# Performance work log

Measured on AMD Instinct MI355X. Metric: run time of the kernel, lower is better.

Reference implementation:

```python
import jax, jax.numpy as jnp
import numpy as np

N, E, B = 30000, 240000, 64
F, H, T = 64, 4, 3
BOT = 256


def _gat_layer(x, e_src, e_dst, lin_w, att_src, att_dst, bias):
    # x: [N, in]; lin_w: [in, H*F]; att_*: [H, F]; bias: [H*F]
    xs = (x @ lin_w).reshape(N, H, F)                     # [N,H,F]
    a_src = jnp.einsum('nhf,hf->nh', xs, att_src)         # [N,H]
    a_dst = jnp.einsum('nhf,hf->nh', xs, att_dst)
    logits = jax.nn.leaky_relu(a_src[e_src] + a_dst[e_dst], negative_slope=0.2)  # [E2,H]
    m = jax.ops.segment_max(logits, e_dst, num_segments=N)        # softmax over in-edges per dst
    ex = jnp.exp(logits - m[e_dst])
    denom = jax.ops.segment_sum(ex, e_dst, num_segments=N)
    alpha = ex / (denom[e_dst] + 1e-16)                   # [E2,H]
    msg = alpha[:, :, None] * xs[e_src]                   # [E2,H,F]
    out = jax.ops.segment_sum(msg, e_dst, num_segments=N).reshape(N, H * F)
    return out + bias


def setup_inputs() -> dict:
    key = jax.random.key(0)
    ks = jax.random.split(key, 20)
    s = 0.1
    inp = {
        'street_feature': jax.random.normal(ks[0], (N, 5), jnp.float32),
        'edge_index': jax.random.randint(ks[1], (2, E), 0, N, dtype=jnp.int64),
        'batch': jnp.sort(jax.random.randint(ks[2], (N,), 0, B, dtype=jnp.int64)),
        'bbox_w': jax.random.normal(ks[3], (5, F), jnp.float32) * s,
        'bbox_b': jnp.zeros((F,), jnp.float32),
        'lin_w0': jax.random.normal(ks[4], (F, H * F), jnp.float32) * s,
        'att_src0': jax.random.normal(ks[5], (H, F), jnp.float32) * s,
        'att_dst0': jax.random.normal(ks[6], (H, F), jnp.float32) * s,
        'bias0': jnp.zeros((H * F,), jnp.float32),
        'lin_w1': jax.random.normal(ks[7], (H * F, H * F), jnp.float32) * s,
        'att_src1': jax.random.normal(ks[8], (H, F), jnp.float32) * s,
        'att_dst1': jax.random.normal(ks[9], (H, F), jnp.float32) * s,
        'bias1': jnp.zeros((H * F,), jnp.float32),
        'lin_w2': jax.random.normal(ks[10], (H * F, H * F), jnp.float32) * s,
        'att_src2': jax.random.normal(ks[11], (H, F), jnp.float32) * s,
        'att_dst2': jax.random.normal(ks[12], (H, F), jnp.float32) * s,
        'bias2': jnp.zeros((H * F,), jnp.float32),
        'agg_w': jax.random.normal(ks[13], (F * (1 + H * T), BOT), jnp.float32) * s,
        'agg_b': jnp.zeros((BOT,), jnp.float32),
    }
    return inp


def reference(street_feature, edge_index, batch,
              bbox_w, bbox_b,
              lin_w0, att_src0, att_dst0, bias0,
              lin_w1, att_src1, att_dst1, bias1,
              lin_w2, att_src2, att_dst2, bias2,
              agg_w, agg_b):
    # add self-loops (PyG GATConv default add_self_loops=True)
    loop = jnp.arange(N, dtype=edge_index.dtype)
    e_src = jnp.concatenate([edge_index[0], loop])
    e_dst = jnp.concatenate([edge_index[1], loop])

    x = jax.nn.relu(street_feature @ bbox_w + bbox_b)            # [N,F]
    g = [jax.ops.segment_max(x, batch, num_segments=B)]          # global max pool

    layers = [(lin_w0, att_src0, att_dst0, bias0),
              (lin_w1, att_src1, att_dst1, bias1),
              (lin_w2, att_src2, att_dst2, bias2)]
    for lw, asrc, adst, b in layers:
        x = jax.nn.relu(_gat_layer(x, e_src, e_dst, lw, asrc, adst, b))  # [N,H*F]
        g.append(jax.ops.segment_max(x, batch, num_segments=B))

    g_embed = jnp.concatenate(g, axis=1)                          # [B, F*(1+H*T)]
    return g_embed @ agg_w + agg_b                                # [B, BOT]
```

## Files before the change

### kernel.cpp

```cpp
#include <hip/hip_runtime.h>
#include <hip/hip_bf16.h>

#define N_NODES 30000
#define N_EDGES 240000
#define NB      64
#define FDIM    64
#define NH      4
#define HF      256
#define E2      (N_EDGES + N_NODES)
#define GCOLS   832
#define BOTD    256
#define DEGCAP  64
#define PSPLIT  16
#define FSPLIT  8

typedef __hip_bfloat16 bf16;
typedef __attribute__((ext_vector_type(8))) short short8;
typedef __attribute__((ext_vector_type(4))) float f32x4;
typedef __attribute__((ext_vector_type(4))) unsigned short u16x4;

__device__ __forceinline__ float b2f(bf16 v) { return __bfloat162float(v); }
__device__ __forceinline__ float bits2f(unsigned short u) {
    return __uint_as_float(((unsigned int)u) << 16);
}

#define ENC_B   7500
#define ADJ_B   1055
#define BOFF_B  118
#define WT0 (HF * FDIM)
#define WT1 (WT0 + HF * HF)
#define WT2 (WT1 + HF * HF)
#define WCONV_B 576
#define GZ_B    208
#define OZ_B    64
#define PRO_B   (ENC_B + ADJ_B + BOFF_B + WCONV_B + GZ_B + OZ_B)

__global__ __launch_bounds__(256) void prologue_kernel(
        const float* __restrict__ sf, const float* __restrict__ bw,
        const float* __restrict__ bb, bf16* __restrict__ xenc,
        const int* __restrict__ esrc, const int* __restrict__ edst,
        int* __restrict__ deg, unsigned short* __restrict__ adj,
        const int* __restrict__ batch, int* __restrict__ boff,
        const float* __restrict__ w0, const float* __restrict__ w1,
        const float* __restrict__ w2, bf16* __restrict__ wT,
        float* __restrict__ g, float* __restrict__ dout) {
    int b = blockIdx.x, t = threadIdx.x;
    if (b < ENC_B) {
        int i = b * 256 + t;
        int n = i >> 6, f = i & 63;
        float acc = bb[f];
#pragma unroll
        for (int k = 0; k < 5; ++k)
            acc += sf[n * 5 + k] * bw[k * FDIM + f];
        xenc[i] = __float2bfloat16(fmaxf(acc, 0.f));
    } else if (b < ENC_B + ADJ_B) {
        int e = (b - ENC_B) * 256 + t;
        if (e >= E2) return;
        int s, d;
        if (e < N_EDGES) { s = esrc[e]; d = edst[e]; }
        else             { s = d = e - N_EDGES; }
        int pos = atomicAdd(&deg[d], 1);
        if (pos < DEGCAP) adj[d * DEGCAP + pos] = (unsigned short)s;
    } else if (b < ENC_B + ADJ_B + BOFF_B) {
        int n = (b - ENC_B - ADJ_B) * 256 + t;
        if (n >= N_NODES) return;
        int b1 = batch[n];
        int b0 = (n == 0) ? -1 : batch[n - 1];
        for (int x = b0 + 1; x <= b1; ++x) boff[x] = n;
        if (n == N_NODES - 1)
            for (int x = b1 + 1; x <= NB; ++x) boff[x] = N_NODES;
    } else if (b < ENC_B + ADJ_B + BOFF_B + WCONV_B) {
        int i = (b - ENC_B - ADJ_B - BOFF_B) * 256 + t;
        if (i < WT0) {
            int n = i / FDIM, k = i - n * FDIM;
            wT[i] = __float2bfloat16(w0[k * HF + n]);
        } else if (i < WT1) {
            int j = i - WT0, n = j >> 8, k = j & 255;
            wT[i] = __float2bfloat16(w1[k * HF + n]);
        } else if (i < WT2) {
            int j = i - WT1, n = j >> 8, k = j & 255;
            wT[i] = __float2bfloat16(w2[k * HF + n]);
        }
    } else if (b < ENC_B + ADJ_B + BOFF_B + WCONV_B + GZ_B) {
        g[(b - ENC_B - ADJ_B - BOFF_B - WCONV_B) * 256 + t] = 0.f;
    } else {
        dout[(b - ENC_B - ADJ_B - BOFF_B - WCONV_B - GZ_B) * 256 + t] = 0.f;
    }
}

template <int K>
__global__ __launch_bounds__(256) void gemm_mfma_kernel(
        const bf16* __restrict__ xb, const bf16* __restrict__ wT,
        bf16* __restrict__ y, const float* __restrict__ asrc,
        const float* __restrict__ adst, float* __restrict__ a_s,
        float* __restrict__ a_d) {
    constexpr int T = K / 32;
    __shared__ __align__(16) short lds[3 * 10240];
    int t = threadIdx.x, w = t >> 6, l = t & 63;
    int q = l >> 4, m = l & 15;
    int n0 = blockIdx.x * 64;
    const short* xg = (const short*)xb;
    const short* wg = (const short*)wT;
    int sub = l >> 2;
    int k2g = (l & 3) ^ ((l >> 3) & 3);
    int xq  = q ^ ((m >> 1) & 3);
    long rowA = n0 + 16 * w + sub;

    auto stage = [&](int s) {
        int bb = s % 3;
        int k0 = s * 32;
        __builtin_amdgcn_global_load_lds(
            (const __attribute__((address_space(1))) void*)&xg[rowA * K + k0 + k2g * 8],
            (__attribute__((address_space(3))) void*)&lds[bb * 10240 + w * 512],
            16, 0, 0);
#pragma unroll
        for (int u = 0; u < 4; ++u) {
            int rowB = 64 * w + 16 * u + sub;
            __builtin_amdgcn_global_load_lds(
                (const __attribute__((address_space(1))) void*)&wg[(long)rowB * K + k0 + k2g * 8],
                (__attribute__((address_space(3))) void*)&lds[bb * 10240 + 2048 + (w * 4 + u) * 512],
                16, 0, 0);
        }
    };

    f32x4 acc[4][4];
#pragma unroll
    for (int rt = 0; rt < 4; ++rt)
#pragma unroll
        for (int ct = 0; ct < 4; ++ct)
            acc[rt][ct] = (f32x4){0.f, 0.f, 0.f, 0.f};

    stage(0);
    if (T > 1) stage(1);

#pragma unroll
    for (int s = 0; s < T; ++s) {
        if (s < T - 1) asm volatile("s_waitcnt vmcnt(5)" ::: "memory");
        else           asm volatile("s_waitcnt vmcnt(0)" ::: "memory");
        __builtin_amdgcn_s_barrier();
        __builtin_amdgcn_sched_barrier(0);
        if (s + 2 < T) stage(s + 2);
        const short* Ab = &lds[(s % 3) * 10240];
        const short* Bb = Ab + 2048;
        short8 af[4], bfr[4];
#pragma unroll
        for (int rt = 0; rt < 4; ++rt)
            af[rt] = *(const short8*)&Ab[(16 * rt + m) * 32 + xq * 8];
#pragma unroll
        for (int ct = 0; ct < 4; ++ct)
            bfr[ct] = *(const short8*)&Bb[(64 * w + 16 * ct + m) * 32 + xq * 8];
#pragma unroll
        for (int rt = 0; rt < 4; ++rt)
#pragma unroll
            for (int ct = 0; ct < 4; ++ct)
                acc[rt][ct] = __builtin_amdgcn_mfma_f32_16x16x32_bf16(
                    af[rt], bfr[ct], acc[rt][ct], 0, 0, 0);
    }

#pragma unroll
    for (int rt = 0; rt < 4; ++rt)
#pragma unroll
        for (int reg = 0; reg < 4; ++reg) {
            int row = n0 + 16 * rt + 4 * q + reg;
            if (row < N_NODES) {
#pragma unroll
                for (int ct = 0; ct < 4; ++ct)
                    y[(long)row * HF + 64 * w + 16 * ct + m] =
                        __float2bfloat16(acc[rt][ct][reg]);
            }
        }
    float vs[4], vd[4];
#pragma unroll
    for (int ct = 0; ct < 4; ++ct) {
        vs[ct] = asrc[64 * w + 16 * ct + m];
        vd[ct] = adst[64 * w + 16 * ct + m];
    }
#pragma unroll
    for (int rt = 0; rt < 4; ++rt)
#pragma unroll
        for (int reg = 0; reg < 4; ++reg) {
            float ps = 0.f, pd = 0.f;
#pragma unroll
            for (int ct = 0; ct < 4; ++ct) {
                ps += acc[rt][ct][reg] * vs[ct];
                pd += acc[rt][ct][reg] * vd[ct];
            }
#pragma unroll
            for (int mask = 1; mask <= 8; mask <<= 1) {
                ps += __shfl_xor(ps, mask, 64);
                pd += __shfl_xor(pd, mask, 64);
            }
            if (m == 0) {
                int row = n0 + 16 * rt + 4 * q + reg;
                if (row < N_NODES) {
                    a_s[row * NH + w] = ps;
                    a_d[row * NH + w] = pd;
                }
            }
        }
}

#define EXP_S (DEGCAP + 4)
__global__ __launch_bounds__(256) void agg_kernel(
        const unsigned short* __restrict__ adj, const int* __restrict__ deg,
        const bf16* __restrict__ xs, const float* __restrict__ a_s,
        const float* __restrict__ a_d, const float* __restrict__ bias,
        bf16* __restrict__ xout) {
    int w = threadIdx.x >> 6, l = threadIdx.x & 63;
    int n = blockIdx.x * 4 + w;
    __shared__ unsigned short s_src_all[4][DEGCAP];
    __shared__ float s_ex_all[4][NH][EXP_S];
    unsigned short* s_src = s_src_all[w];
    float (*s_ex)[EXP_S] = s_ex_all[w];
    int dn = min(deg[n], DEGCAP);
    int src_l = 0;
    if (l < dn) {
        src_l = adj[n * DEGCAP + l];
        s_src[l] = (unsigned short)src_l;
    }
    f32x4 ad4 = *(const f32x4*)&a_d[n * NH];
    float ex[NH];
    if (l < dn) {
        f32x4 as4 = *(const f32x4*)&a_s[src_l * NH];
#pragma unroll
        for (int h = 0; h < NH; ++h) {
            float a = as4[h] + ad4[h];
            a = (a > 0.f) ? a : 0.2f * a;
            ex[h] = __expf(a);
        }
    } else {
#pragma unroll
        for (int h = 0; h < NH; ++h) ex[h] = 0.f;
    }
#pragma unroll
    for (int h = 0; h < NH; ++h) {
        float s = ex[h];
#pragma unroll
        for (int off = 32; off > 0; off >>= 1) s += __shfl_xor(s, off, 64);
        s_ex[h][l] = ex[h] * (1.f / (s + 1e-16f));
    }
    __builtin_amdgcn_wave_barrier();
    int hh = l >> 4;
    const unsigned short* xg = (const unsigned short*)xs;
    f32x4 acc = {0.f, 0.f, 0.f, 0.f};
    int k = 0;
    for (; k + 1 < dn; k += 2) {
        int s0 = s_src[k], s1 = s_src[k + 1];
        float a0 = s_ex[hh][k], a1 = s_ex[hh][k + 1];
        u16x4 v0 = *(const u16x4*)&xg[(long)s0 * HF + 4 * l];
        u16x4 v1 = *(const u16x4*)&xg[(long)s1 * HF + 4 * l];
#pragma unroll
        for (int j = 0; j < 4; ++j) {
            acc[j] += a0 * bits2f(v0[j]);
            acc[j] += a1 * bits2f(v1[j]);
        }
    }
    if (k < dn) {
        int s0 = s_src[k];
        float a0 = s_ex[hh][k];
        u16x4 v0 = *(const u16x4*)&xg[(long)s0 * HF + 4 * l];
#pragma unroll
        for (int j = 0; j < 4; ++j) acc[j] += a0 * bits2f(v0[j]);
    }
    f32x4 b4 = *(const f32x4*)&bias[4 * l];
    u16x4 o;
#pragma unroll
    for (int j = 0; j < 4; ++j) {
        bf16 ob = __float2bfloat16(fmaxf(acc[j] + b4[j], 0.f));
        o[j] = *reinterpret_cast<unsigned short*>(&ob);
    }
    *(u16x4*)((unsigned short*)xout + (long)n * HF + 4 * l) = o;
}

__global__ __launch_bounds__(256) void pool256_kernel(const bf16* __restrict__ x,
                                                      const int* __restrict__ boff,
                                                      unsigned int* __restrict__ g, int goff) {
    int b = blockIdx.x / PSPLIT, part = blockIdx.x % PSPLIT;
    int t = threadIdx.x, w = t >> 6, l = t & 63;
    int s = boff[b], e = boff[b + 1];
    int chunk = (e - s + PSPLIT - 1) / PSPLIT;
    int cs = s + part * chunk, ce = min(cs + chunk, e);
    if (cs >= ce) return;
    __shared__ f32x4 sm[256];
    const unsigned short* xg = (const unsigned short*)x;
    f32x4 v = {0.f, 0.f, 0.f, 0.f};
    for (int n = cs + w; n < ce; n += 4) {
        u16x4 u = *(const u16x4*)&xg[(long)n * HF + 4 * l];
#pragma unroll
        for (int j = 0; j < 4; ++j) v[j] = fmaxf(v[j], bits2f(u[j]));
    }
    sm[t] = v;
    __syncthreads();
    const float* smf = (const float*)sm;
    float m = fmaxf(fmaxf(smf[t], smf[256 + t]), fmaxf(smf[512 + t], smf[768 + t]));
    atomicMax(&g[b * GCOLS + goff + t], __float_as_uint(m));
}

__global__ __launch_bounds__(256) void pool64_kernel(const bf16* __restrict__ x,
                                                     const int* __restrict__ boff,
                                                     unsigned int* __restrict__ g) {
    int b = blockIdx.x / PSPLIT, part = blockIdx.x % PSPLIT;
    int t = threadIdx.x, c = t & 63, r = t >> 6;
    int s = boff[b], e = boff[b + 1];
    int chunk = (e - s + PSPLIT - 1) / PSPLIT;
    int cs = s + part * chunk, ce = min(cs + chunk, e);
    __shared__ float sm[256];
    float v = 0.f;
    for (int n = cs + r; n < ce; n += 4)
        v = fmaxf(v, b2f(x[(long)n * FDIM + c]));
    sm[t] = v;
    __syncthreads();
    if (t < 64 && cs < ce) {
        float m = fmaxf(fmaxf(sm[t], sm[t + 64]), fmaxf(sm[t + 128], sm[t + 192]));
        atomicMax(&g[b * GCOLS + t], __float_as_uint(m));
    }
}

__global__ __launch_bounds__(256) void final_kernel(
        const float* __restrict__ g, const float* __restrict__ w,
        const float* __restrict__ b, float* __restrict__ outp) {
    int bb = blockIdx.x & (NB - 1);
    int slice = blockIdx.x >> 6;
    int j = threadIdx.x;
    const int KS = GCOLS / FSPLIT;
    float acc = (slice == 0) ? b[j] : 0.f;
    int k0 = slice * KS;
    for (int k = k0; k < k0 + KS; ++k)
        acc += g[bb * GCOLS + k] * w[k * BOTD + j];
    atomicAdd(&outp[bb * BOTD + j], acc);
}

extern "C" void kernel_launch(void* const* d_in, const int* in_sizes, int n_in,
                              void* d_out, int out_size, void* d_ws, size_t ws_size,
                              hipStream_t stream) {
    const float* sf     = (const float*)d_in[0];
    const int*   eidx   = (const int*)d_in[1];
    const int*   batch  = (const int*)d_in[2];
    const float* bbox_w = (const float*)d_in[3];
    const float* bbox_b = (const float*)d_in[4];
    const float* lin_w[3] = {(const float*)d_in[5],  (const float*)d_in[9],  (const float*)d_in[13]};
    const float* att_s[3] = {(const float*)d_in[6],  (const float*)d_in[10], (const float*)d_in[14]};
    const float* att_d[3] = {(const float*)d_in[7],  (const float*)d_in[11], (const float*)d_in[15]};
    const float* bias[3]  = {(const float*)d_in[8],  (const float*)d_in[12], (const float*)d_in[16]};
    const float* agg_w  = (const float*)d_in[17];
    const float* agg_b  = (const float*)d_in[18];

    const int* esrc = eidx;
    const int* edst = eidx + N_EDGES;

    char* ws = (char*)d_ws;
    bf16* xsb  = (bf16*)ws;  ws += (size_t)N_NODES * HF * 2;
    bf16* xb0  = (bf16*)ws;  ws += (size_t)N_NODES * HF * 2;
    bf16* xb1  = (bf16*)ws;  ws += (size_t)N_NODES * HF * 2;
    bf16* xenc = (bf16*)ws;  ws += (size_t)N_NODES * FDIM * 2;
    float* a_s = (float*)ws; ws += (size_t)N_NODES * NH * 4;
    float* a_d = (float*)ws; ws += (size_t)N_NODES * NH * 4;
    float* g   = (float*)ws; ws += (size_t)NB * GCOLS * 4;
    int*   deg = (int*)ws;   ws += (size_t)N_NODES * 4;
    int*   boff= (int*)ws;   ws += (size_t)(NB + 1) * 4;
    unsigned short* adj = (unsigned short*)ws; ws += (size_t)N_NODES * DEGCAP * 2;
    bf16* wT   = (bf16*)ws;  ws += (size_t)WT2 * 2;

    hipMemsetAsync(deg, 0, (size_t)N_NODES * 4, stream);
    prologue_kernel<<<PRO_B, 256, 0, stream>>>(
        sf, bbox_w, bbox_b, xenc, esrc, edst, deg, adj, batch, boff,
        lin_w[0], lin_w[1], lin_w[2], wT, g, (float*)d_out);
    pool64_kernel<<<NB * PSPLIT, 256, 0, stream>>>(xenc, boff, (unsigned int*)g);

    const bf16* wTl[3] = {wT, wT + WT0, wT + WT1};
    const bf16* xin = xenc;
    bf16* xout = xb0;
    for (int l = 0; l < 3; ++l) {
        if (l == 0)
            gemm_mfma_kernel<FDIM><<<(N_NODES + 63) / 64, 256, 0, stream>>>(
                xin, wTl[l], xsb, att_s[l], att_d[l], a_s, a_d);
        else
            gemm_mfma_kernel<HF><<<(N_NODES + 63) / 64, 256, 0, stream>>>(
                xin, wTl[l], xsb, att_s[l], att_d[l], a_s, a_d);
        agg_kernel<<<N_NODES / 4, 256, 0, stream>>>(adj, deg, xsb, a_s, a_d, bias[l], xout);
        pool256_kernel<<<NB * PSPLIT, 256, 0, stream>>>(xout, boff, (unsigned int*)g, FDIM + l * HF);
        xin = xout;
        xout = (xout == xb0) ? xb1 : xb0;
    }
    final_kernel<<<NB * FSPLIT, 256, 0, stream>>>(g, agg_w, agg_b, (float*)d_out);
}
```

Measured before the change: 276.4 us.

## Fuse encoder max-pool into prologue, memset g/out, unroll aggregation by four

The first global max-pool over the encoded features moves into the prologue's encoder blocks. Each block reduces its four nodes in shared memory and issues atomicMax into g, which removes the separate pool64 kernel launch. The zeroing of g and the output is replaced by memsets, with g placed right after deg so a single memset covers both. The edge aggregation loop is unrolled from two to four gathers per iteration to put more loads in flight. The cost is extra atomics and a __syncthreads in the encoder path, and the pool now depends on g being zeroed before the prologue runs.

```diff
diff --git a/kernel.cpp b/kernel.cpp
--- a/kernel.cpp
+++ b/kernel.cpp
@@ -31,9 +31,7 @@
 #define WT1 (WT0 + HF * HF)
 #define WT2 (WT1 + HF * HF)
 #define WCONV_B 576
-#define GZ_B    208
-#define OZ_B    64
-#define PRO_B   (ENC_B + ADJ_B + BOFF_B + WCONV_B + GZ_B + OZ_B)
+#define PRO_B   (ENC_B + ADJ_B + BOFF_B + WCONV_B)
 
 __global__ __launch_bounds__(256) void prologue_kernel(
         const float* __restrict__ sf, const float* __restrict__ bw,
@@ -43,16 +41,34 @@
         const int* __restrict__ batch, int* __restrict__ boff,
         const float* __restrict__ w0, const float* __restrict__ w1,
         const float* __restrict__ w2, bf16* __restrict__ wT,
-        float* __restrict__ g, float* __restrict__ dout) {
+        unsigned int* __restrict__ g) {
+    __shared__ float s_pool[4][FDIM];
     int b = blockIdx.x, t = threadIdx.x;
     if (b < ENC_B) {
         int i = b * 256 + t;
-        int n = i >> 6, f = i & 63;
+        int n = i >> 6, f = i & 63, w = t >> 6;
         float acc = bb[f];
 #pragma unroll
         for (int k = 0; k < 5; ++k)
             acc += sf[n * 5 + k] * bw[k * FDIM + f];
-        xenc[i] = __float2bfloat16(fmaxf(acc, 0.f));
+        bf16 ob = __float2bfloat16(fmaxf(acc, 0.f));
+        xenc[i] = ob;
+        s_pool[w][f] = b2f(ob);
+        __syncthreads();
+        int n0b = b * 4;
+        int bA = batch[n0b], bB = batch[n0b + 3];
+        if (t < FDIM) {
+            if (bA == bB) {
+                float m = fmaxf(fmaxf(s_pool[0][t], s_pool[1][t]),
+                                fmaxf(s_pool[2][t], s_pool[3][t]));
+                atomicMax(&g[bA * GCOLS + t], __float_as_uint(m));
+            } else {
+#pragma unroll
+                for (int ww = 0; ww < 4; ++ww)
+                    atomicMax(&g[batch[n0b + ww] * GCOLS + t],
+                              __float_as_uint(s_pool[ww][t]));
+            }
+        }
     } else if (b < ENC_B + ADJ_B) {
         int e = (b - ENC_B) * 256 + t;
         if (e >= E2) return;
@@ -69,7 +85,7 @@
         for (int x = b0 + 1; x <= b1; ++x) boff[x] = n;
         if (n == N_NODES - 1)
             for (int x = b1 + 1; x <= NB; ++x) boff[x] = N_NODES;
-    } else if (b < ENC_B + ADJ_B + BOFF_B + WCONV_B) {
+    } else {
         int i = (b - ENC_B - ADJ_B - BOFF_B) * 256 + t;
         if (i < WT0) {
             int n = i / FDIM, k = i - n * FDIM;
@@ -81,10 +97,6 @@
             int j = i - WT1, n = j >> 8, k = j & 255;
             wT[i] = __float2bfloat16(w2[k * HF + n]);
         }
-    } else if (b < ENC_B + ADJ_B + BOFF_B + WCONV_B + GZ_B) {
-        g[(b - ENC_B - ADJ_B - BOFF_B - WCONV_B) * 256 + t] = 0.f;
-    } else {
-        dout[(b - ENC_B - ADJ_B - BOFF_B - WCONV_B - GZ_B) * 256 + t] = 0.f;
     }
 }
 
@@ -241,23 +253,30 @@
     }
     __builtin_amdgcn_wave_barrier();
     int hh = l >> 4;
+    const float* exh = s_ex[hh];
     const unsigned short* xg = (const unsigned short*)xs;
     f32x4 acc = {0.f, 0.f, 0.f, 0.f};
     int k = 0;
-    for (; k + 1 < dn; k += 2) {
-        int s0 = s_src[k], s1 = s_src[k + 1];
-        float a0 = s_ex[hh][k], a1 = s_ex[hh][k + 1];
+    for (; k + 3 < dn; k += 4) {
+        int s0 = s_src[k],     s1 = s_src[k + 1];
+        int s2 = s_src[k + 2], s3 = s_src[k + 3];
+        float a0 = exh[k],     a1 = exh[k + 1];
+        float a2 = exh[k + 2], a3 = exh[k + 3];
         u16x4 v0 = *(const u16x4*)&xg[(long)s0 * HF + 4 * l];
         u16x4 v1 = *(const u16x4*)&xg[(long)s1 * HF + 4 * l];
+        u16x4 v2 = *(const u16x4*)&xg[(long)s2 * HF + 4 * l];
+        u16x4 v3 = *(const u16x4*)&xg[(long)s3 * HF + 4 * l];
 #pragma unroll
         for (int j = 0; j < 4; ++j) {
             acc[j] += a0 * bits2f(v0[j]);
             acc[j] += a1 * bits2f(v1[j]);
-        }
-    }
-    if (k < dn) {
+            acc[j] += a2 * bits2f(v2[j]);
+            acc[j] += a3 * bits2f(v3[j]);
+        }
+    }
+    for (; k < dn; ++k) {
         int s0 = s_src[k];
-        float a0 = s_ex[hh][k];
+        float a0 = exh[k];
         u16x4 v0 = *(const u16x4*)&xg[(long)s0 * HF + 4 * l];
 #pragma unroll
         for (int j = 0; j < 4; ++j) acc[j] += a0 * bits2f(v0[j]);
@@ -296,26 +315,6 @@
     atomicMax(&g[b * GCOLS + goff + t], __float_as_uint(m));
 }
 
-__global__ __launch_bounds__(256) void pool64_kernel(const bf16* __restrict__ x,
-                                                     const int* __restrict__ boff,
-                                                     unsigned int* __restrict__ g) {
-    int b = blockIdx.x / PSPLIT, part = blockIdx.x % PSPLIT;
-    int t = threadIdx.x, c = t & 63, r = t >> 6;
-    int s = boff[b], e = boff[b + 1];
-    int chunk = (e - s + PSPLIT - 1) / PSPLIT;
-    int cs = s + part * chunk, ce = min(cs + chunk, e);
-    __shared__ float sm[256];
-    float v = 0.f;
-    for (int n = cs + r; n < ce; n += 4)
-        v = fmaxf(v, b2f(x[(long)n * FDIM + c]));
-    sm[t] = v;
-    __syncthreads();
-    if (t < 64 && cs < ce) {
-        float m = fmaxf(fmaxf(sm[t], sm[t + 64]), fmaxf(sm[t + 128], sm[t + 192]));
-        atomicMax(&g[b * GCOLS + t], __float_as_uint(m));
-    }
-}
-
 __global__ __launch_bounds__(256) void final_kernel(
         const float* __restrict__ g, const float* __restrict__ w,
         const float* __restrict__ b, float* __restrict__ outp) {
@@ -355,17 +354,17 @@
     bf16* xenc = (bf16*)ws;  ws += (size_t)N_NODES * FDIM * 2;
     float* a_s = (float*)ws; ws += (size_t)N_NODES * NH * 4;
     float* a_d = (float*)ws; ws += (size_t)N_NODES * NH * 4;
+    int*   deg = (int*)ws;   ws += (size_t)N_NODES * 4;
     float* g   = (float*)ws; ws += (size_t)NB * GCOLS * 4;
-    int*   deg = (int*)ws;   ws += (size_t)N_NODES * 4;
-    int*   boff= (int*)ws;   ws += (size_t)(NB + 1) * 4;
+    int*   boff= (int*)ws;   ws += 1024;
     unsigned short* adj = (unsigned short*)ws; ws += (size_t)N_NODES * DEGCAP * 2;
     bf16* wT   = (bf16*)ws;  ws += (size_t)WT2 * 2;
 
-    hipMemsetAsync(deg, 0, (size_t)N_NODES * 4, stream);
+    hipMemsetAsync(deg, 0, (size_t)N_NODES * 4 + (size_t)NB * GCOLS * 4, stream);
+    hipMemsetAsync(d_out, 0, (size_t)NB * BOTD * 4, stream);
     prologue_kernel<<<PRO_B, 256, 0, stream>>>(
         sf, bbox_w, bbox_b, xenc, esrc, edst, deg, adj, batch, boff,
-        lin_w[0], lin_w[1], lin_w[2], wT, g, (float*)d_out);
-    pool64_kernel<<<NB * PSPLIT, 256, 0, stream>>>(xenc, boff, (unsigned int*)g);
+        lin_w[0], lin_w[1], lin_w[2], wT, (unsigned int*)g);
 
     const bf16* wTl[3] = {wT, wT + WT0, wT + WT1};
     const bf16* xin = xenc;
```

After: 274.9 us. About the same (-0.6%).
